# Kernel optimization log

Hardware: AMD Instinct MI355X
Metric: run time of the kernel (lower is better)

Reference implementation:

```python
import jax, jax.numpy as jnp
import numpy as np

D = 768          # emb_dim (BERT hidden size)
N_DOM = 9        # domain_num
N_EXP = 6        # num_expert (per-domain)
N_SH = 4         # num_shared_expert
N_TOT = N_EXP + N_SH  # total experts seen by the gate
B = 2048


def _p(key, shape, scale=0.02):
    return jax.random.normal(key, shape, dtype=jnp.float32) * scale


def setup_inputs() -> dict:
    key = jax.random.key(0)
    ks = jax.random.split(key, 32)
    inp = {
        "content_pooled": jax.random.normal(ks[0], (B, D), dtype=jnp.float32),
        "ftr_pooled": jax.random.normal(ks[1], (B, D), dtype=jnp.float32),
        "category": jax.random.randint(ks[2], (B,), 0, N_DOM, dtype=jnp.int64),
        "domain_emb": _p(ks[3], (N_DOM, D), 1.0),
    }
    # per-domain expert stacks: Linear(D,D)-SiLU-Linear(D,D), for content (c) and ftr (f)
    for pre, base in (("c", 4), ("f", 12)):
        inp[pre + "W1"] = _p(ks[base + 0], (N_DOM, N_EXP, D, D))
        inp[pre + "b1"] = jnp.zeros((N_DOM, N_EXP, D), jnp.float32)
        inp[pre + "W2"] = _p(ks[base + 1], (N_DOM, N_EXP, D, D))
        inp[pre + "b2"] = jnp.zeros((N_DOM, N_EXP, D), jnp.float32)
        # shared experts: Linear(D,D)-SiLU-Linear(D,D)
        inp[pre + "sW1"] = _p(ks[base + 2], (N_SH, D, D))
        inp[pre + "sb1"] = jnp.zeros((N_SH, D), jnp.float32)
        inp[pre + "sW2"] = _p(ks[base + 3], (N_SH, D, D))
        inp[pre + "sb2"] = jnp.zeros((N_SH, D), jnp.float32)
        # per-domain enhanced gates: Linear(2D,D)-SiLU-Linear(D,N_TOT), temperature scalar per domain
        inp[pre + "gW1"] = _p(ks[base + 4], (N_DOM, 2 * D, D))
        inp[pre + "gb1"] = jnp.zeros((N_DOM, D), jnp.float32)
        inp[pre + "gW2"] = _p(ks[base + 5], (N_DOM, D, N_TOT))
        inp[pre + "gb2"] = jnp.zeros((N_DOM, N_TOT), jnp.float32)
        inp[pre + "temp"] = jnp.ones((N_DOM,), jnp.float32)
    return inp


def _moe_branch(x, category, domain_emb, W1, b1, W2, b2,
                sW1, sb1, sW2, sb2, gW1, gb1, gW2, gb2, temp):
    # x: [B, D]; category: [B] int in [0, N_DOM)
    demb = domain_emb[category]                           # [B, D]
    g_in = jnp.concatenate([demb, x], axis=-1)            # [B, 2D]
    # gate computed for all domains, then per-example domain selected
    gh = jax.nn.silu(jnp.einsum("bx,nxh->bnh", g_in, gW1) + gb1)      # [B, 9, D]
    logits = jnp.einsum("bnh,nhe->bne", gh, gW2) + gb2                 # [B, 9, 10]
    t = jax.nn.softplus(temp) + 1e-4                                    # positive temperature
    gates_all = jax.nn.softmax(logits / t[None, :, None], axis=-1)
    gates = jnp.take_along_axis(gates_all, category[:, None, None], axis=1)[:, 0]  # [B, 10]
    # per-domain experts for all domains (grouped GEMM form), then select domain
    h1 = jax.nn.silu(jnp.einsum("bd,nedh->bneh", x, W1) + b1)          # [B, 9, 6, D]
    e_all = jnp.einsum("bneh,nehd->bned", h1, W2) + b2                 # [B, 9, 6, D]
    e_dom = jnp.take_along_axis(e_all, category[:, None, None, None], axis=1)[:, 0]  # [B, 6, D]
    # shared experts
    hs = jax.nn.silu(jnp.einsum("bd,edh->beh", x, sW1) + sb1)          # [B, 4, D]
    e_sh = jnp.einsum("beh,ehd->bed", hs, sW2) + sb2                   # [B, 4, D]
    experts = jnp.concatenate([e_dom, e_sh], axis=1)                   # [B, 10, D]
    return jnp.einsum("be,bed->bd", gates, experts)                    # [B, D]


def reference(content_pooled, ftr_pooled, category, domain_emb,
              cW1, cb1, cW2, cb2, csW1, csb1, csW2, csb2,
              cgW1, cgb1, cgW2, cgb2, ctemp,
              fW1, fb1, fW2, fb2, fsW1, fsb1, fsW2, fsb2,
              fgW1, fgb1, fgW2, fgb2, ftemp):
    c_out = _moe_branch(content_pooled, category, domain_emb,
                        cW1, cb1, cW2, cb2, csW1, csb1, csW2, csb2,
                        cgW1, cgb1, cgW2, cgb2, ctemp)
    f_out = _moe_branch(ftr_pooled, category, domain_emb,
                        fW1, fb1, fW2, fb2, fsW1, fsb1, fsW2, fsb2,
                        fgW1, fgb1, fgW2, fgb2, ftemp)
    return jnp.concatenate([c_out, f_out], axis=-1)  # [B, 2D]
```

## Files before the change

kernel.cpp:

```cpp
#include <hip/hip_runtime.h>

#define D_ 768
#define B_ 2048
#define NDOM 9
#define NTOT 10
#define MT 128
#define NT 128
#define KT 32
#define KI1 (D_ / KT)

#define E2   589824ull
#define E2G  1179648ull
#define OFF_WT2 31850496ull
#define OFF_SW1 63700992ull
#define OFF_SW2 66060288ull
#define OFF_GW1 68419584ull
#define ZWE     79036416ull

typedef _Float16 f16;
typedef _Float16 f16x8 __attribute__((ext_vector_type(8)));
typedef _Float16 f16x4 __attribute__((ext_vector_type(4)));
typedef _Float16 f16x2 __attribute__((ext_vector_type(2)));
typedef float f32x4 __attribute__((ext_vector_type(4)));

typedef const __attribute__((address_space(1))) void gas_void;
typedef __attribute__((address_space(3))) void las_void;

__device__ __forceinline__ void gload16(const f16* g, f16* l) {
  __builtin_amdgcn_global_load_lds((gas_void*)g, (las_void*)l, 16, 0, 0);
}

#define WAITV4() asm volatile("s_waitcnt vmcnt(4)" ::: "memory")
#define WAITV0() asm volatile("s_waitcnt vmcnt(0)" ::: "memory")
#define SBAR()   do { __builtin_amdgcn_s_barrier(); __builtin_amdgcn_sched_barrier(0); } while (0)

__global__ __launch_bounds__(256) void bucket_kernel(const int* cat32, int* perm,
                                                     int* off, int* cnt, int* dom) {
  __shared__ int scnt[NDOM], soff[NDOM], scur[NDOM];
  __shared__ int odd_nz;
  int t = threadIdx.x;
  if (t == 0) odd_nz = 0;
  if (t < NDOM) scnt[t] = 0;
  __syncthreads();
  int loc = 0;
  for (int i = t; i < B_; i += 256)
    if ((i & 1) && cat32[i] != 0) loc = 1;
  if (loc) atomicOr(&odd_nz, 1);
  __syncthreads();
  int strd = odd_nz ? 1 : 2;
  for (int i = t; i < B_; i += 256) atomicAdd(&scnt[cat32[i * strd]], 1);
  __syncthreads();
  if (t == 0) { int a = 0; for (int n = 0; n < NDOM; n++) { soff[n] = a; a += scnt[n]; } }
  __syncthreads();
  if (t < NDOM) { scur[t] = soff[t]; off[t] = soff[t]; cnt[t] = scnt[t]; }
  __syncthreads();
  for (int i = t; i < B_; i += 256) {
    int n = cat32[i * strd];
    int pos = atomicAdd(&scur[n], 1);
    perm[pos] = i;
    dom[pos] = n;
  }
}

__global__ __launch_bounds__(256) void cvt_kernel(const float* src, f16* dst, int n8) {
  int i = blockIdx.x * 256 + threadIdx.x;
  if (i >= n8) return;
  const f32x4* s = (const f32x4*)(src + (size_t)i * 8);
  f32x4 a = s[0], b = s[1];
  f16x8 o;
  o[0]=(f16)a[0]; o[1]=(f16)a[1]; o[2]=(f16)a[2]; o[3]=(f16)a[3];
  o[4]=(f16)b[0]; o[5]=(f16)b[1]; o[6]=(f16)b[2]; o[7]=(f16)b[3];
  *(f16x8*)(dst + (size_t)i * 8) = o;
}

struct TRP { const float* s[10]; f16* wt; };

__global__ __launch_bounds__(256) void trans_kernel(TRP p) {
  const int m = blockIdx.z, z = m / 125, r = m % 125;
  const float* src; f16* dst; int R;
  const size_t zw = (size_t)z * ZWE;
  if (r < 54)       { src = p.s[0+z] + (size_t)r*E2;        dst = p.wt + zw + (size_t)r*E2;                 R = 768; }
  else if (r < 108) { int i=r-54;  src = p.s[2+z] + (size_t)i*E2;  dst = p.wt + zw + OFF_WT2 + (size_t)i*E2;  R = 768; }
  else if (r < 112) { int i=r-108; src = p.s[4+z] + (size_t)i*E2;  dst = p.wt + zw + OFF_SW1 + (size_t)i*E2;  R = 768; }
  else if (r < 116) { int i=r-112; src = p.s[6+z] + (size_t)i*E2;  dst = p.wt + zw + OFF_SW2 + (size_t)i*E2;  R = 768; }
  else              { int i=r-116; src = p.s[8+z] + (size_t)i*E2G; dst = p.wt + zw + OFF_GW1 + (size_t)i*E2G; R = 1536; }
  const int ty = blockIdx.y;
  if (ty * 64 >= R) return;
  const int tx = blockIdx.x;

  __shared__ f16 tile[64][76];
  const int t = threadIdx.x;
  const int lr = t >> 4, lc = (t & 15) * 4;
#pragma unroll
  for (int i = 0; i < 4; i++) {
    int row = lr + i * 16;
    f32x4 v = *(const f32x4*)(src + (size_t)(ty*64 + row) * 768 + tx*64 + lc);
    tile[lc+0][row] = (f16)v[0];
    tile[lc+1][row] = (f16)v[1];
    tile[lc+2][row] = (f16)v[2];
    tile[lc+3][row] = (f16)v[3];
  }
  __syncthreads();
  const int orow = t >> 3, oc = (t & 7) * 8;
#pragma unroll
  for (int i = 0; i < 2; i++) {
    int r2 = orow + i * 32;
    union { f16x8 v8; f16x4 v4[2]; } u;
    u.v4[0] = *(const f16x4*)&tile[r2][oc];
    u.v4[1] = *(const f16x4*)&tile[r2][oc + 4];
    *(f16x8*)(dst + (size_t)(tx*64 + r2) * R + ty*64 + oc) = u.v8;
  }
}

struct L1P {
  const f16* x16[2]; const f16* demb16; const f16* wt;
  const float* b1[2]; const float* sb1[2]; const float* gb1[2];
  const int* perm; const int* off; const int* cnt;
  f16* h;
};

#define NBL1 3792
#define QX1  474

__global__ __launch_bounds__(256, 3) void layer1_kernel(L1P p) {
  const int raw = blockIdx.x;
  const int L = (raw & 7) * QX1 + (raw >> 3);
  const int z = L / 1896;
  const int rem = L - z * 1896;
  const int g = rem / 24;
  const int x = rem % 24;
  const int nt = x % 6;
  int mt0 = x / 6, mtstep = 4;

  int row_off, row_cnt, slot, gdom = 0, kiters = KI1;
  const f16* WT; const float* bias;
  bool isGate = false;
  const size_t zw = (size_t)z * ZWE;
  if (g < 54) {
    int n = g / 6, e = g % 6;
    row_off = p.off[n]; row_cnt = p.cnt[n];
    WT = p.wt + zw + (size_t)(n*6+e) * E2;
    bias = p.b1[z] + (n*6+e) * D_;
    slot = e;
  } else if (g < 70) {
    int s_ = g - 54, e = s_ >> 2;
    row_off = 0; row_cnt = B_;
    WT = p.wt + zw + OFF_SW1 + (size_t)e * E2;
    bias = p.sb1[z] + e * D_;
    slot = 6 + e;
    mt0 = x / 6 + 4 * (s_ & 3); mtstep = 16;
  } else {
    int n = g - 70;
    row_off = p.off[n]; row_cnt = p.cnt[n];
    WT = p.wt + zw + OFF_GW1 + (size_t)n * E2G;
    bias = p.gb1[z] + n * D_;
    slot = 10; isGate = true; gdom = n; kiters = 2 * KI1;
  }
  const int KW = isGate ? 2 * D_ : D_;

  __shared__ f16 As[3][MT][KT];
  __shared__ f16 Bs[3][MT][KT];

  const int t = threadIdx.x;
  const int wave = t >> 6, lane = t & 63;
  const int wr = (wave >> 1) * 64, wc = (wave & 1) * 64;
  const int r0 = lane & 15, q = lane >> 4;
  const int jbase = nt * NT;
  const int lrow = lane >> 2;
  const int lk = 8 * ((lane & 3) ^ ((lane >> 3) & 3));
  const int qa = (q ^ ((r0 >> 1) & 3)) * 8;

  const f16* bBase[2];
#pragma unroll
  for (int i = 0; i < 2; i++) {
    int col = jbase + 32 * wave + 16 * i + lrow;
    bBase[i] = WT + (size_t)col * KW + lk;
  }
  const f16* dB = p.demb16 + (size_t)gdom * D_ + lk;

  for (int mt = mt0; mt * MT < row_cnt; mt += mtstep) {
    const f16* aBase[2];
#pragma unroll
    for (int i = 0; i < 2; i++) {
      int rl = mt * MT + 32 * wave + 16 * i + lrow;
      int pr = p.perm[(rl < row_cnt) ? (row_off + rl) : row_off];
      aBase[i] = p.x16[z] + (size_t)pr * D_ + lk;
    }

    auto STAGE = [&](int buf, int kk) {
      const int k0 = kk * KT;
#pragma unroll
      for (int i = 0; i < 2; i++) {
        const f16* as;
        if (isGate) as = (k0 < D_) ? (dB + k0) : (aBase[i] + (k0 - D_));
        else        as = aBase[i] + k0;
        gload16(as, &As[buf][32 * wave + 16 * i][0]);
        gload16(bBase[i] + k0, &Bs[buf][32 * wave + 16 * i][0]);
      }
    };

    f32x4 acc[4][4];
#pragma unroll
    for (int a = 0; a < 4; a++)
#pragma unroll
      for (int b = 0; b < 4; b++) acc[a][b] = (f32x4){0.f, 0.f, 0.f, 0.f};

    STAGE(0, 0);
    STAGE(1, 1);
    WAITV4();
    SBAR();

    int cur = 0;
    for (int kk = 0; kk < kiters; kk++) {
      int pf = cur + 2; if (pf >= 3) pf -= 3;
      if (kk + 2 < kiters) STAGE(pf, kk + 2);
      f16x8 af[4], bf[4];
#pragma unroll
      for (int m = 0; m < 4; m++) af[m] = *(const f16x8*)&As[cur][wr + m * 16 + r0][qa];
#pragma unroll
      for (int nn = 0; nn < 4; nn++) bf[nn] = *(const f16x8*)&Bs[cur][wc + nn * 16 + r0][qa];
      __builtin_amdgcn_s_setprio(1);
#pragma unroll
      for (int m = 0; m < 4; m++)
#pragma unroll
        for (int nn = 0; nn < 4; nn++)
          acc[m][nn] = __builtin_amdgcn_mfma_f32_16x16x32_f16(af[m], bf[nn], acc[m][nn], 0, 0, 0);
      __builtin_amdgcn_s_setprio(0);
      if (kk + 2 < kiters) { WAITV4(); } else { WAITV0(); }
      SBAR();
      cur = (cur == 2) ? 0 : cur + 1;
    }

    f16* hout = p.h + (size_t)(z * 11 + slot) * B_ * D_;
#pragma unroll
    for (int nn = 0; nn < 4; nn++) {
      const int col = jbase + wc + nn * 16 + r0;
      const float bc = bias[col];
#pragma unroll
      for (int m = 0; m < 4; m++) {
#pragma unroll
        for (int i = 0; i < 4; i++) {
          int lr = mt * MT + wr + m * 16 + q * 4 + i;
          if (lr < row_cnt) {
            float v = acc[m][nn][i] + bc;
            v = v / (1.f + __expf(-v));
            hout[(size_t)(row_off + lr) * D_ + col] = (f16)v;
          }
        }
      }
    }
  }
}

struct GP {
  const f16* h;
  const float* gW2[2]; const float* gb2[2]; const float* temp[2];
  const int* dom;
  float* gates;
};

__global__ __launch_bounds__(256) void gate_kernel(GP p) {
  int wid = (blockIdx.x * 256 + threadIdx.x) >> 6;
  int lane = threadIdx.x & 63;
  int z = wid >> 11;
  int pos = wid & (B_ - 1);
  int n = p.dom[pos];
  const f16* gh = p.h + ((size_t)(z * 11 + 10) * B_ + pos) * D_;
  const float* W = p.gW2[z] + (size_t)n * D_ * NTOT;
  float part[NTOT];
#pragma unroll
  for (int e = 0; e < NTOT; e++) part[e] = 0.f;
  for (int k = lane; k < D_; k += 64) {
    float a = (float)gh[k];
    const float* wrow = W + (size_t)k * NTOT;
#pragma unroll
    for (int e = 0; e < NTOT; e++) part[e] = fmaf(a, wrow[e], part[e]);
  }
#pragma unroll
  for (int e = 0; e < NTOT; e++) {
    float v = part[e];
#pragma unroll
    for (int s = 32; s > 0; s >>= 1) v += __shfl_xor(v, s, 64);
    part[e] = v;
  }
  float tv = p.temp[z][n];
  float tq = (tv > 15.f ? tv : log1pf(__expf(tv))) + 1e-4f;
  const float* b2 = p.gb2[z] + n * NTOT;
  float mx = -1e30f;
#pragma unroll
  for (int e = 0; e < NTOT; e++) { part[e] = (part[e] + b2[e]) / tq; mx = fmaxf(mx, part[e]); }
  float s = 0.f;
#pragma unroll
  for (int e = 0; e < NTOT; e++) { part[e] = __expf(part[e] - mx); s += part[e]; }
  float inv = 1.f / s;
  if (lane < NTOT) p.gates[((size_t)z * B_ + pos) * NTOT + lane] = part[lane] * inv;
}

struct L2P {
  const f16* h; const f16* wt;
  const float* b2[2]; const float* sb2[2];
  const float* gates;
  const int* perm; const int* off; const int* cnt;
  float* out;
};

#define NBL2 2160
#define QX2  270

__global__ __launch_bounds__(256, 3) void layer2_kernel(L2P p) {
  const int raw = blockIdx.x;
  const int L = (raw & 7) * QX2 + (raw >> 3);
  const int zz = L / 216;
  const int rem = L % 216;
  const int n = rem / 24;
  const int x = rem % 24;
  const int z = zz / 5, es = zz % 5, ebase = es * 2;
  const int nt = x % 6, mt0 = x / 6;
  const int row_off = p.off[n], row_cnt = p.cnt[n];

  __shared__ f16 As[3][MT][KT];
  __shared__ f16 Bs[3][MT][KT];
  __shared__ float sg[MT][2];
  __shared__ int sperm[MT];

  const int t = threadIdx.x;
  const int wave = t >> 6, lane = t & 63;
  const int wr = (wave >> 1) * 64, wc = (wave & 1) * 64;
  const int r0 = lane & 15, q = lane >> 4;
  const int jbase = nt * NT;
  const int lrow = lane >> 2;
  const int lk = 8 * ((lane & 3) ^ ((lane >> 3) & 3));
  const int qa = (q ^ ((r0 >> 1) & 3)) * 8;

  const size_t zw = (size_t)z * ZWE;
  const f16* WB0; const f16* WB1; const float* pb[2]; size_t slotOff[2];
  {
    int e0 = ebase, e1 = ebase + 1;
    WB0 = (e0 < 6) ? (p.wt + zw + OFF_WT2 + (size_t)(n*6+e0)*E2) : (p.wt + zw + OFF_SW2 + (size_t)(e0-6)*E2);
    WB1 = (e1 < 6) ? (p.wt + zw + OFF_WT2 + (size_t)(n*6+e1)*E2) : (p.wt + zw + OFF_SW2 + (size_t)(e1-6)*E2);
    pb[0] = (e0 < 6) ? (p.b2[z] + (size_t)(n*6+e0)*D_) : (p.sb2[z] + (size_t)(e0-6)*D_);
    pb[1] = (e1 < 6) ? (p.b2[z] + (size_t)(n*6+e1)*D_) : (p.sb2[z] + (size_t)(e1-6)*D_);
    slotOff[0] = (size_t)(z*11 + e0) * B_ * D_;
    slotOff[1] = (size_t)(z*11 + e1) * B_ * D_;
  }

  const f16* bB0[2]; const f16* bB1[2];
#pragma unroll
  for (int i = 0; i < 2; i++) {
    int col = jbase + 32 * wave + 16 * i + lrow;
    bB0[i] = WB0 + (size_t)col * D_ + lk;
    bB1[i] = WB1 + (size_t)col * D_ + lk;
  }

  for (int mt = mt0; mt * MT < row_cnt; mt += 4) {
    for (int i = t; i < MT * 2; i += 256) {
      int rr = i >> 1, e = i & 1;
      int gp = row_off + mt * MT + rr;
      sg[rr][e] = (gp < B_ && (mt * MT + rr) < row_cnt)
                  ? p.gates[((size_t)z * B_ + gp) * NTOT + ebase + e] : 0.f;
    }
    for (int i = t; i < MT; i += 256) {
      int gp = row_off + mt * MT + i;
      sperm[i] = (gp < B_) ? p.perm[gp] : 0;
    }
    __syncthreads();

    const f16* aB0[2]; const f16* aB1[2];
#pragma unroll
    for (int i = 0; i < 2; i++) {
      int rl = mt * MT + 32 * wave + 16 * i + lrow;
      int rr = (rl < row_cnt) ? (row_off + rl) : row_off;
      size_t rp = (size_t)rr * D_ + lk;
      aB0[i] = p.h + slotOff[0] + rp;
      aB1[i] = p.h + slotOff[1] + rp;
    }
    f16 gA[4], gB[4];
#pragma unroll
    for (int m = 0; m < 4; m++) {
      gA[m] = (f16)sg[wr + m * 16 + r0][0];
      gB[m] = (f16)sg[wr + m * 16 + r0][1];
    }

    auto STAGE = [&](int buf, int it) {
      const int ei = (it >= KI1);
      const int k0 = (it - (ei ? KI1 : 0)) * KT;
#pragma unroll
      for (int i = 0; i < 2; i++) {
        const f16* as = (ei ? aB1[i] : aB0[i]) + k0;
        const f16* bs = (ei ? bB1[i] : bB0[i]) + k0;
        gload16(as, &As[buf][32 * wave + 16 * i][0]);
        gload16(bs, &Bs[buf][32 * wave + 16 * i][0]);
      }
    };

    f32x4 acc[4][4];
#pragma unroll
    for (int a = 0; a < 4; a++)
#pragma unroll
      for (int b = 0; b < 4; b++) acc[a][b] = (f32x4){0.f, 0.f, 0.f, 0.f};

    const int total = 2 * KI1;
    STAGE(0, 0);
    STAGE(1, 1);
    WAITV4();
    SBAR();

    int cur = 0;
    for (int it = 0; it < total; it++) {
      int pf = cur + 2; if (pf >= 3) pf -= 3;
      if (it + 2 < total) STAGE(pf, it + 2);
      const int ei = (it >= KI1);
      f16x8 af[4], bf[4];
#pragma unroll
      for (int m = 0; m < 4; m++) {
        af[m] = *(const f16x8*)&As[cur][wr + m * 16 + r0][qa];
        af[m] = af[m] * (ei ? gB[m] : gA[m]);
      }
#pragma unroll
      for (int nn = 0; nn < 4; nn++) bf[nn] = *(const f16x8*)&Bs[cur][wc + nn * 16 + r0][qa];
      __builtin_amdgcn_s_setprio(1);
#pragma unroll
      for (int m = 0; m < 4; m++)
#pragma unroll
        for (int nn = 0; nn < 4; nn++)
          acc[m][nn] = __builtin_amdgcn_mfma_f32_16x16x32_f16(af[m], bf[nn], acc[m][nn], 0, 0, 0);
      __builtin_amdgcn_s_setprio(0);
      if (it + 2 < total) { WAITV4(); } else { WAITV0(); }
      SBAR();
      cur = (cur == 2) ? 0 : cur + 1;
    }

    const int zoff = z * D_;
#pragma unroll
    for (int nn = 0; nn < 4; nn++) {
      const int col = jbase + wc + nn * 16 + r0;
      float pbc0 = pb[0][col], pbc1 = pb[1][col];
#pragma unroll
      for (int m = 0; m < 4; m++) {
#pragma unroll
        for (int i = 0; i < 4; i++) {
          const int lrt = wr + m * 16 + q * 4 + i;
          if (mt * MT + lrt < row_cnt) {
            float v = acc[m][nn][i];
            v = fmaf(sg[lrt][0], pbc0, v);
            v = fmaf(sg[lrt][1], pbc1, v);
            float* dst = p.out + (size_t)sperm[lrt] * (2 * D_) + zoff + col;
            __hip_atomic_fetch_add(dst, v, __ATOMIC_RELAXED, __HIP_MEMORY_SCOPE_AGENT);
          }
        }
      }
    }
    __syncthreads();
  }
}

extern "C" void kernel_launch(void* const* d_in, const int* in_sizes, int n_in,
                              void* d_out, int out_size, void* d_ws, size_t ws_size,
                              hipStream_t stream) {
  const float* content = (const float*)d_in[0];
  const float* ftr     = (const float*)d_in[1];
  const int*   cat     = (const int*)d_in[2];
  const float* demb    = (const float*)d_in[3];

  const float* cW1  = (const float*)d_in[4];
  const float* cb1  = (const float*)d_in[5];
  const float* cW2  = (const float*)d_in[6];
  const float* cb2  = (const float*)d_in[7];
  const float* csW1 = (const float*)d_in[8];
  const float* csb1 = (const float*)d_in[9];
  const float* csW2 = (const float*)d_in[10];
  const float* csb2 = (const float*)d_in[11];
  const float* cgW1 = (const float*)d_in[12];
  const float* cgb1 = (const float*)d_in[13];
  const float* cgW2 = (const float*)d_in[14];
  const float* cgb2 = (const float*)d_in[15];
  const float* ctemp= (const float*)d_in[16];

  const float* fW1  = (const float*)d_in[17];
  const float* fb1  = (const float*)d_in[18];
  const float* fW2  = (const float*)d_in[19];
  const float* fb2  = (const float*)d_in[20];
  const float* fsW1 = (const float*)d_in[21];
  const float* fsb1 = (const float*)d_in[22];
  const float* fsW2 = (const float*)d_in[23];
  const float* fsb2 = (const float*)d_in[24];
  const float* fgW1 = (const float*)d_in[25];
  const float* fgb1 = (const float*)d_in[26];
  const float* fgW2 = (const float*)d_in[27];
  const float* fgb2 = (const float*)d_in[28];
  const float* ftemp= (const float*)d_in[29];

  char* wsb = (char*)d_ws;
  int* perm    = (int*)wsb;
  int* off     = (int*)(wsb + 8192);
  int* cnt     = (int*)(wsb + 8256);
  int* dom     = (int*)(wsb + 8320);
  float* gates = (float*)(wsb + 16512);
  f16* h       = (f16*)(wsb + 180352);
  f16* x16a    = (f16*)(wsb + 69386368);
  f16* x16b    = (f16*)(wsb + 72532096);
  f16* demb16  = (f16*)(wsb + 75677824);
  f16* wt      = (f16*)(wsb + 75691648);
  float* out   = (float*)d_out;

  (void)hipMemsetAsync(d_out, 0, (size_t)out_size * sizeof(float), stream);

  bucket_kernel<<<1, 256, 0, stream>>>(cat, perm, off, cnt, dom);

  cvt_kernel<<<768, 256, 0, stream>>>(content, x16a, (B_ * D_) / 8);
  cvt_kernel<<<768, 256, 0, stream>>>(ftr, x16b, (B_ * D_) / 8);
  cvt_kernel<<<4, 256, 0, stream>>>(demb, demb16, (NDOM * D_) / 8);

  TRP tp;
  tp.s[0] = cW1;  tp.s[1] = fW1;
  tp.s[2] = cW2;  tp.s[3] = fW2;
  tp.s[4] = csW1; tp.s[5] = fsW1;
  tp.s[6] = csW2; tp.s[7] = fsW2;
  tp.s[8] = cgW1; tp.s[9] = fgW1;
  tp.wt = wt;
  trans_kernel<<<dim3(12, 24, 250), 256, 0, stream>>>(tp);

  L1P p1;
  p1.x16[0] = x16a; p1.x16[1] = x16b; p1.demb16 = demb16; p1.wt = wt;
  p1.b1[0] = cb1;  p1.b1[1] = fb1;
  p1.sb1[0] = csb1; p1.sb1[1] = fsb1;
  p1.gb1[0] = cgb1; p1.gb1[1] = fgb1;
  p1.perm = perm; p1.off = off; p1.cnt = cnt; p1.h = h;
  layer1_kernel<<<dim3(NBL1), 256, 0, stream>>>(p1);

  GP pg;
  pg.h = h; pg.gW2[0] = cgW2; pg.gW2[1] = fgW2;
  pg.gb2[0] = cgb2; pg.gb2[1] = fgb2;
  pg.temp[0] = ctemp; pg.temp[1] = ftemp;
  pg.dom = dom; pg.gates = gates;
  gate_kernel<<<dim3((2 * B_) / 4), 256, 0, stream>>>(pg);

  L2P p2;
  p2.h = h; p2.wt = wt;
  p2.b2[0] = cb2;  p2.b2[1] = fb2;
  p2.sb2[0] = csb2; p2.sb2[1] = fsb2;
  p2.gates = gates; p2.perm = perm; p2.off = off; p2.cnt = cnt; p2.out = out;
  layer2_kernel<<<dim3(NBL2), 256, 0, stream>>>(p2);

  (void)in_sizes; (void)n_in; (void)ws_size;
}
```

Before: 582.3 us.

## Load A operands directly from global into registers, drop A LDS staging

```diff
diff --git a/kernel.cpp b/kernel.cpp
--- a/kernel.cpp
+++ b/kernel.cpp
@@ -19,7 +19,6 @@
 
 typedef _Float16 f16;
 typedef _Float16 f16x8 __attribute__((ext_vector_type(8)));
-typedef _Float16 f16x4 __attribute__((ext_vector_type(4)));
 typedef _Float16 f16x2 __attribute__((ext_vector_type(2)));
 typedef float f32x4 __attribute__((ext_vector_type(4)));
 
@@ -30,9 +29,12 @@
   __builtin_amdgcn_global_load_lds((gas_void*)g, (las_void*)l, 16, 0, 0);
 }
 
-#define WAITV4() asm volatile("s_waitcnt vmcnt(4)" ::: "memory")
+#define WAITV2() asm volatile("s_waitcnt vmcnt(2)" ::: "memory")
 #define WAITV0() asm volatile("s_waitcnt vmcnt(0)" ::: "memory")
 #define SBAR()   do { __builtin_amdgcn_s_barrier(); __builtin_amdgcn_sched_barrier(0); } while (0)
+#define SCHED0() __builtin_amdgcn_sched_barrier(0)
+
+struct AF { f16x8 v[4]; };
 
 __global__ __launch_bounds__(256) void bucket_kernel(const int* cat32, int* perm,
                                                      int* off, int* cnt, int* dom) {
@@ -88,27 +90,29 @@
   if (ty * 64 >= R) return;
   const int tx = blockIdx.x;
 
-  __shared__ f16 tile[64][76];
+  __shared__ float tile[64][65];
   const int t = threadIdx.x;
   const int lr = t >> 4, lc = (t & 15) * 4;
 #pragma unroll
   for (int i = 0; i < 4; i++) {
     int row = lr + i * 16;
     f32x4 v = *(const f32x4*)(src + (size_t)(ty*64 + row) * 768 + tx*64 + lc);
-    tile[lc+0][row] = (f16)v[0];
-    tile[lc+1][row] = (f16)v[1];
-    tile[lc+2][row] = (f16)v[2];
-    tile[lc+3][row] = (f16)v[3];
+    tile[lc+0][row] = v[0];
+    tile[lc+1][row] = v[1];
+    tile[lc+2][row] = v[2];
+    tile[lc+3][row] = v[3];
   }
   __syncthreads();
   const int orow = t >> 3, oc = (t & 7) * 8;
 #pragma unroll
   for (int i = 0; i < 2; i++) {
     int r2 = orow + i * 32;
-    union { f16x8 v8; f16x4 v4[2]; } u;
-    u.v4[0] = *(const f16x4*)&tile[r2][oc];
-    u.v4[1] = *(const f16x4*)&tile[r2][oc + 4];
-    *(f16x8*)(dst + (size_t)(tx*64 + r2) * R + ty*64 + oc) = u.v8;
+    f32x4 a = *(const f32x4*)&tile[r2][oc];
+    f32x4 b = *(const f32x4*)&tile[r2][oc + 4];
+    f16x8 o;
+    o[0]=(f16)a[0]; o[1]=(f16)a[1]; o[2]=(f16)a[2]; o[3]=(f16)a[3];
+    o[4]=(f16)b[0]; o[5]=(f16)b[1]; o[6]=(f16)b[2]; o[7]=(f16)b[3];
+    *(f16x8*)(dst + (size_t)(tx*64 + r2) * R + ty*64 + oc) = o;
   }
 }
 
@@ -158,7 +162,6 @@
   }
   const int KW = isGate ? 2 * D_ : D_;
 
-  __shared__ f16 As[3][MT][KT];
   __shared__ f16 Bs[3][MT][KT];
 
   const int t = threadIdx.x;
@@ -176,27 +179,35 @@
     int col = jbase + 32 * wave + 16 * i + lrow;
     bBase[i] = WT + (size_t)col * KW + lk;
   }
-  const f16* dB = p.demb16 + (size_t)gdom * D_ + lk;
+  const f16* dP = p.demb16 + (size_t)gdom * D_ + q * 8;
 
   for (int mt = mt0; mt * MT < row_cnt; mt += mtstep) {
-    const f16* aBase[2];
-#pragma unroll
-    for (int i = 0; i < 2; i++) {
-      int rl = mt * MT + 32 * wave + 16 * i + lrow;
+    const f16* aP[4];
+#pragma unroll
+    for (int m = 0; m < 4; m++) {
+      int rl = mt * MT + wr + m * 16 + r0;
       int pr = p.perm[(rl < row_cnt) ? (row_off + rl) : row_off];
-      aBase[i] = p.x16[z] + (size_t)pr * D_ + lk;
-    }
-
+      aP[m] = p.x16[z] + (size_t)pr * D_ + q * 8;
+    }
+
+    AF afA, afB;
+    auto LOADA = [&](int kk, AF& d) {
+      const int k0 = kk * KT;
+      if (isGate && k0 < D_) {
+        f16x8 vv = *(const f16x8*)(dP + k0);
+#pragma unroll
+        for (int m = 0; m < 4; m++) d.v[m] = vv;
+      } else {
+        const int ko = k0 - (isGate ? D_ : 0);
+#pragma unroll
+        for (int m = 0; m < 4; m++) d.v[m] = *(const f16x8*)(aP[m] + ko);
+      }
+    };
     auto STAGE = [&](int buf, int kk) {
       const int k0 = kk * KT;
 #pragma unroll
-      for (int i = 0; i < 2; i++) {
-        const f16* as;
-        if (isGate) as = (k0 < D_) ? (dB + k0) : (aBase[i] + (k0 - D_));
-        else        as = aBase[i] + k0;
-        gload16(as, &As[buf][32 * wave + 16 * i][0]);
+      for (int i = 0; i < 2; i++)
         gload16(bBase[i] + k0, &Bs[buf][32 * wave + 16 * i][0]);
-      }
     };
 
     f32x4 acc[4][4];
@@ -205,28 +216,42 @@
 #pragma unroll
       for (int b = 0; b < 4; b++) acc[a][b] = (f32x4){0.f, 0.f, 0.f, 0.f};
 
+    auto COMPUTE = [&](int buf, const AF& a) {
+      f16x8 bf[4];
+#pragma unroll
+      for (int nn = 0; nn < 4; nn++) bf[nn] = *(const f16x8*)&Bs[buf][wc + nn * 16 + r0][qa];
+      __builtin_amdgcn_s_setprio(1);
+#pragma unroll
+      for (int m = 0; m < 4; m++)
+#pragma unroll
+        for (int nn = 0; nn < 4; nn++)
+          acc[m][nn] = __builtin_amdgcn_mfma_f32_16x16x32_f16(a.v[m], bf[nn], acc[m][nn], 0, 0, 0);
+      __builtin_amdgcn_s_setprio(0);
+    };
+
+    LOADA(0, afA);
+    SCHED0();
     STAGE(0, 0);
     STAGE(1, 1);
-    WAITV4();
+    WAITV2();
     SBAR();
 
     int cur = 0;
-    for (int kk = 0; kk < kiters; kk++) {
-      int pf = cur + 2; if (pf >= 3) pf -= 3;
-      if (kk + 2 < kiters) STAGE(pf, kk + 2);
-      f16x8 af[4], bf[4];
-#pragma unroll
-      for (int m = 0; m < 4; m++) af[m] = *(const f16x8*)&As[cur][wr + m * 16 + r0][qa];
-#pragma unroll
-      for (int nn = 0; nn < 4; nn++) bf[nn] = *(const f16x8*)&Bs[cur][wc + nn * 16 + r0][qa];
-      __builtin_amdgcn_s_setprio(1);
-#pragma unroll
-      for (int m = 0; m < 4; m++)
-#pragma unroll
-        for (int nn = 0; nn < 4; nn++)
-          acc[m][nn] = __builtin_amdgcn_mfma_f32_16x16x32_f16(af[m], bf[nn], acc[m][nn], 0, 0, 0);
-      __builtin_amdgcn_s_setprio(0);
-      if (kk + 2 < kiters) { WAITV4(); } else { WAITV0(); }
+    for (int kk = 0; kk < kiters; kk += 2) {
+      if (kk + 1 < kiters) LOADA(kk + 1, afB);
+      SCHED0();
+      { int pf = cur + 2; if (pf >= 3) pf -= 3; if (kk + 2 < kiters) STAGE(pf, kk + 2); }
+      SCHED0();
+      COMPUTE(cur, afA);
+      if (kk + 2 < kiters) { WAITV2(); } else { WAITV0(); }
+      SBAR();
+      cur = (cur == 2) ? 0 : cur + 1;
+      if (kk + 2 < kiters) LOADA(kk + 2, afA);
+      SCHED0();
+      { int pf = cur + 2; if (pf >= 3) pf -= 3; if (kk + 3 < kiters) STAGE(pf, kk + 3); }
+      SCHED0();
+      COMPUTE(cur, afB);
+      if (kk + 3 < kiters) { WAITV2(); } else { WAITV0(); }
       SBAR();
       cur = (cur == 2) ? 0 : cur + 1;
     }
@@ -318,7 +343,6 @@
   const int nt = x % 6, mt0 = x / 6;
   const int row_off = p.off[n], row_cnt = p.cnt[n];
 
-  __shared__ f16 As[3][MT][KT];
   __shared__ f16 Bs[3][MT][KT];
   __shared__ float sg[MT][2];
   __shared__ int sperm[MT];
@@ -365,67 +389,81 @@
     }
     __syncthreads();
 
-    const f16* aB0[2]; const f16* aB1[2];
-#pragma unroll
-    for (int i = 0; i < 2; i++) {
-      int rl = mt * MT + 32 * wave + 16 * i + lrow;
+    const f16* aP0[4]; const f16* aP1[4];
+    f16 gA[4], gB[4];
+#pragma unroll
+    for (int m = 0; m < 4; m++) {
+      int rl = mt * MT + wr + m * 16 + r0;
       int rr = (rl < row_cnt) ? (row_off + rl) : row_off;
-      size_t rp = (size_t)rr * D_ + lk;
-      aB0[i] = p.h + slotOff[0] + rp;
-      aB1[i] = p.h + slotOff[1] + rp;
-    }
-    f16 gA[4], gB[4];
-#pragma unroll
-    for (int m = 0; m < 4; m++) {
+      size_t rp = (size_t)rr * D_ + q * 8;
+      aP0[m] = p.h + slotOff[0] + rp;
+      aP1[m] = p.h + slotOff[1] + rp;
       gA[m] = (f16)sg[wr + m * 16 + r0][0];
       gB[m] = (f16)sg[wr + m * 16 + r0][1];
     }
 
+    AF afA, afB;
+    auto LOADA = [&](int it, AF& d) {
+      const int ei = (it >= KI1);
+      const int ko = (it - (ei ? KI1 : 0)) * KT;
+#pragma unroll
+      for (int m = 0; m < 4; m++)
+        d.v[m] = *(const f16x8*)((ei ? aP1[m] : aP0[m]) + ko);
+    };
     auto STAGE = [&](int buf, int it) {
       const int ei = (it >= KI1);
       const int k0 = (it - (ei ? KI1 : 0)) * KT;
 #pragma unroll
-      for (int i = 0; i < 2; i++) {
-        const f16* as = (ei ? aB1[i] : aB0[i]) + k0;
-        const f16* bs = (ei ? bB1[i] : bB0[i]) + k0;
-        gload16(as, &As[buf][32 * wave + 16 * i][0]);
-        gload16(bs, &Bs[buf][32 * wave + 16 * i][0]);
+      for (int i = 0; i < 2; i++)
+        gload16((ei ? bB1[i] : bB0[i]) + k0, &Bs[buf][32 * wave + 16 * i][0]);
+    };
+
+    f32x4 acc[4][4];
+#pragma unroll
+    for (int a = 0; a < 4; a++)
+#pragma unroll
+      for (int b = 0; b < 4; b++) acc[a][b] = (f32x4){0.f, 0.f, 0.f, 0.f};
+
+    auto COMPUTE = [&](int buf, const AF& a, int ei) {
+      f16x8 bf[4];
+#pragma unroll
+      for (int nn = 0; nn < 4; nn++) bf[nn] = *(const f16x8*)&Bs[buf][wc + nn * 16 + r0][qa];
+      __builtin_amdgcn_s_setprio(1);
+#pragma unroll
+      for (int m = 0; m < 4; m++) {
+        f16x8 av = a.v[m] * (ei ? gB[m] : gA[m]);
+#pragma unroll
+        for (int nn = 0; nn < 4; nn++)
+          acc[m][nn] = __builtin_amdgcn_mfma_f32_16x16x32_f16(av, bf[nn], acc[m][nn], 0, 0, 0);
       }
+      __builtin_amdgcn_s_setprio(0);
     };
 
-    f32x4 acc[4][4];
-#pragma unroll
-    for (int a = 0; a < 4; a++)
-#pragma unroll
-      for (int b = 0; b < 4; b++) acc[a][b] = (f32x4){0.f, 0.f, 0.f, 0.f};
-
     const int total = 2 * KI1;
+    LOADA(0, afA);
+    SCHED0();
     STAGE(0, 0);
     STAGE(1, 1);
-    WAITV4();
+    WAITV2();
     SBAR();
 
     int cur = 0;
-    for (int it = 0; it < total; it++) {
-      int pf = cur + 2; if (pf >= 3) pf -= 3;
-      if (it + 2 < total) STAGE(pf, it + 2);
-      const int ei = (it >= KI1);
-      f16x8 af[4], bf[4];
-#pragma unroll
-      for (int m = 0; m < 4; m++) {
-        af[m] = *(const f16x8*)&As[cur][wr + m * 16 + r0][qa];
-        af[m] = af[m] * (ei ? gB[m] : gA[m]);
-      }
-#pragma unroll
-      for (int nn = 0; nn < 4; nn++) bf[nn] = *(const f16x8*)&Bs[cur][wc + nn * 16 + r0][qa];
-      __builtin_amdgcn_s_setprio(1);
-#pragma unroll
-      for (int m = 0; m < 4; m++)
-#pragma unroll
-        for (int nn = 0; nn < 4; nn++)
-          acc[m][nn] = __builtin_amdgcn_mfma_f32_16x16x32_f16(af[m], bf[nn], acc[m][nn], 0, 0, 0);
-      __builtin_amdgcn_s_setprio(0);
-      if (it + 2 < total) { WAITV4(); } else { WAITV0(); }
+    for (int it = 0; it < total; it += 2) {
+      if (it + 1 < total) LOADA(it + 1, afB);
+      SCHED0();
+      { int pf = cur + 2; if (pf >= 3) pf -= 3; if (it + 2 < total) STAGE(pf, it + 2); }
+      SCHED0();
+      COMPUTE(cur, afA, it >= KI1);
+      if (it + 2 < total) { WAITV2(); } else { WAITV0(); }
+      SBAR();
+      cur = (cur == 2) ? 0 : cur + 1;
+
+      if (it + 2 < total) LOADA(it + 2, afA);
+      SCHED0();
+      { int pf = cur + 2; if (pf >= 3) pf -= 3; if (it + 3 < total) STAGE(pf, it + 3); }
+      SCHED0();
+      COMPUTE(cur, afB, (it + 1) >= KI1);
+      if (it + 3 < total) { WAITV2(); } else { WAITV0(); }
       SBAR();
       cur = (cur == 2) ? 0 : cur + 1;
     }
```

Result: slower. 664.2 us (+14.1%).
